# Kernel optimization log

Measured on AMD Instinct MI355X. Metric: run time of the kernel, lower is better.

The kernel has to match this reference:

```python
import math
import jax, jax.numpy as jnp
import numpy as np

FACTOR = 5

def setup_inputs() -> dict:
    key = jax.random.key(0)
    kq, kk, kv, ki = jax.random.split(key, 4)
    b, h, L, d = 4, 8, 4096, 64
    sample_k = min(L, int(FACTOR * math.log(L + 1)))  # 41
    q = jax.random.normal(kq, (b, h, L, d), dtype=jnp.float32)
    k = jax.random.normal(kk, (b, h, L, d), dtype=jnp.float32)
    v = jax.random.normal(kv, (b, h, L, d), dtype=jnp.float32)
    index_sample = jax.random.randint(ki, (L, sample_k), 0, L, dtype=jnp.int64)
    return {"q": q, "k": k, "v": v, "index_sample": index_sample}

def reference(q, k, v, index_sample):
    b, h, l_q, d = q.shape
    l_k = k.shape[2]
    n_top = min(l_q, int(FACTOR * math.log(l_q + 1)))
    # --- ProbSparse query selection ---
    # k_sample[b,h,q,s,d] = k[b,h,index_sample[q,s],d]  (avoids the O(lq*lk*d) expand)
    k_sample = k[:, :, index_sample, :]                      # (b,h,l_q,sample_k,d)
    qk_sample = jnp.einsum('bhqd,bhqsd->bhqs', q, k_sample)  # (b,h,l_q,sample_k)
    m = qk_sample.max(axis=-1) - qk_sample.mean(axis=-1)     # sparsity measure
    _, top_q = jax.lax.top_k(m, n_top)                       # (b,h,n_top)
    # --- sparse attention on selected queries ---
    q_reduce = jnp.take_along_axis(q, top_q[..., None], axis=2)  # (b,h,n_top,d)
    scale = 1.0 / math.sqrt(d)
    scores = jnp.einsum('bhnd,bhkd->bhnk', q_reduce, k) * scale
    attn = jax.nn.softmax(scores, axis=-1)
    context_top = jnp.einsum('bhnk,bhkd->bhnd', attn, v)
    # --- scatter into mean-initialized context (attn_mask is None path) ---
    context = jnp.broadcast_to(v.mean(axis=2, keepdims=True), (b, h, l_q, d))
    bi = jnp.arange(b)[:, None, None]
    hi = jnp.arange(h)[None, :, None]
    context = context.at[bi, hi, top_q].set(context_top)
    return context
```

## Files before the change

### kernel.cpp

```cpp
#include <hip/hip_runtime.h>
#include <hip/hip_bf16.h>


#define NTOP 41
#define NPAD 48
#define CH 64
#define CAND_CAP 64

typedef __attribute__((ext_vector_type(8))) short bf16x8;
typedef __attribute__((ext_vector_type(4))) float f32x4;

__device__ __forceinline__ unsigned short f2bf(float f) {
    unsigned int x = __float_as_uint(f);
    unsigned int r = (x + 0x7FFFu + ((x >> 16) & 1u)) >> 16;
    return (unsigned short)r;
}
__device__ __forceinline__ unsigned int pack2(float lo, float hi) {
    return ((unsigned int)f2bf(hi) << 16) | f2bf(lo);
}
__device__ __forceinline__ float dot8(const float4& qa, const float4& qb,
                                      const float4& ka, const float4& kb) {
    float p = 0.f;
    p = fmaf(qa.x, ka.x, p); p = fmaf(qa.y, ka.y, p);
    p = fmaf(qa.z, ka.z, p); p = fmaf(qa.w, ka.w, p);
    p = fmaf(qb.x, kb.x, p); p = fmaf(qb.y, kb.y, p);
    p = fmaf(qb.z, kb.z, p); p = fmaf(qb.w, kb.w, p);
    return p;
}
__device__ __forceinline__ float red8(float p) {
    p += __shfl_xor(p, 1);
    p += __shfl_xor(p, 2);
    p += __shfl_xor(p, 4);
    return p;
}

__global__ __launch_bounds__(256) void kA_scores(const float* __restrict__ q,
                                                 const float* __restrict__ k,
                                                 const int* __restrict__ idxs,
                                                 float* __restrict__ m_out) {
    __shared__ int sidx[32 * 41];
    int t = threadIdx.x;
    int lane = t & 63, w = t >> 6;
    int g = lane >> 3, sl = lane & 7;
    int lb = ((blockIdx.x & 7) << 9) + (blockIdx.x >> 3);
    long long qflat = (long long)lb * 32 + w * 8 + g;
    int bh = (int)(qflat >> 12);
    int qi0 = (lb * 32) & 4095;
    for (int i = t; i < 32 * 41; i += 256)
        sidx[i] = idxs[(long long)qi0 * 41 + i] & 4095;
    const float4* q4 = (const float4*)q;
    const float4* k4 = (const float4*)k;
    float4 qa = q4[qflat * 16 + sl * 2];
    float4 qb = q4[qflat * 16 + sl * 2 + 1];
    long long kbase = ((long long)bh << 12) * 16;
    __syncthreads();
    const int* irow = sidx + (w * 8 + g) * 41;
    float maxv = -1e30f, sum = 0.f;
#pragma unroll 2
    for (int g4 = 0; g4 < 10; g4++) {
        int ki0 = irow[g4 * 4 + 0], ki1 = irow[g4 * 4 + 1];
        int ki2 = irow[g4 * 4 + 2], ki3 = irow[g4 * 4 + 3];
        float4 ka0 = k4[kbase + (long long)ki0 * 16 + sl * 2];
        float4 kb0 = k4[kbase + (long long)ki0 * 16 + sl * 2 + 1];
        float4 ka1 = k4[kbase + (long long)ki1 * 16 + sl * 2];
        float4 kb1 = k4[kbase + (long long)ki1 * 16 + sl * 2 + 1];
        float4 ka2 = k4[kbase + (long long)ki2 * 16 + sl * 2];
        float4 kb2 = k4[kbase + (long long)ki2 * 16 + sl * 2 + 1];
        float4 ka3 = k4[kbase + (long long)ki3 * 16 + sl * 2];
        float4 kb3 = k4[kbase + (long long)ki3 * 16 + sl * 2 + 1];
        float p0 = red8(dot8(qa, qb, ka0, kb0));
        float p1 = red8(dot8(qa, qb, ka1, kb1));
        float p2 = red8(dot8(qa, qb, ka2, kb2));
        float p3 = red8(dot8(qa, qb, ka3, kb3));
        maxv = fmaxf(maxv, fmaxf(fmaxf(p0, p1), fmaxf(p2, p3)));
        sum += (p0 + p1) + (p2 + p3);
    }
    {
        int ki = irow[40];
        float4 ka = k4[kbase + (long long)ki * 16 + sl * 2];
        float4 kb = k4[kbase + (long long)ki * 16 + sl * 2 + 1];
        float p = red8(dot8(qa, qb, ka, kb));
        maxv = fmaxf(maxv, p);
        sum += p;
    }
    if (sl == 0) m_out[qflat] = maxv - sum * (1.0f / 41.0f);
}

__global__ __launch_bounds__(256) void kB_topk(const float* __restrict__ m_in,
                                               int* __restrict__ topq) {
    __shared__ unsigned int uvals[4096];
    __shared__ unsigned int hist[256];
    __shared__ unsigned int scal[4];
    __shared__ int candIdx[CAND_CAP];
    __shared__ unsigned int candU[CAND_CAP];
    int bh = blockIdx.x, t = threadIdx.x;
    for (int i = t; i < 4096; i += 256) {
        unsigned int b = __float_as_uint(m_in[bh * 4096 + i]);
        uvals[i] = (b & 0x80000000u) ? ~b : (b | 0x80000000u);
    }
    hist[t] = 0;
    __syncthreads();
    for (int i = t; i < 4096; i += 256) atomicAdd(&hist[uvals[i] >> 24], 1u);
    __syncthreads();
    if (t == 0) {
        unsigned int cum = 0, b1 = 0, ca = 0;
        for (int j = 255; j >= 0; j--) {
            if (cum + hist[j] >= 41u) { b1 = (unsigned)j; ca = cum; break; }
            cum += hist[j];
        }
        scal[0] = b1; scal[1] = ca;
    }
    __syncthreads();
    unsigned int b1 = scal[0];
    hist[t] = 0;
    __syncthreads();
    for (int i = t; i < 4096; i += 256)
        if ((uvals[i] >> 24) == b1) atomicAdd(&hist[(uvals[i] >> 16) & 255u], 1u);
    __syncthreads();
    if (t == 0) {
        unsigned int cum = scal[1], b2 = 0;
        for (int j = 255; j >= 0; j--) {
            if (cum + hist[j] >= 41u) { b2 = (unsigned)j; break; }
            cum += hist[j];
        }
        scal[2] = (b1 << 24) | (b2 << 16);
        scal[3] = 0;
    }
    __syncthreads();
    unsigned int T = scal[2];
    for (int i = t; i < 4096; i += 256) {
        unsigned int u = uvals[i];
        if (u >= T) {
            unsigned int pos = atomicAdd(&scal[3], 1u);
            if (pos < CAND_CAP) { candIdx[pos] = i; candU[pos] = u; }
        }
    }
    __syncthreads();
    if (t < 64) {
        int n = (int)min(scal[3], (unsigned)CAND_CAP);
        unsigned int myU = (t < n) ? candU[t] : 0u;
        int myI = (t < n) ? candIdx[t] : 0x7fffffff;
        for (int it = 0; it < NTOP; it++) {
            unsigned int bu = myU;
            int bi = myI;
            for (int off = 32; off; off >>= 1) {
                unsigned int ou = __shfl_xor(bu, off);
                int oi = __shfl_xor(bi, off);
                if (ou > bu || (ou == bu && oi < bi)) { bu = ou; bi = oi; }
            }
            if (t == 0) topq[bh * NTOP + it] = bi;
            if (myI == bi) { myU = 0u; myI = 0x7fffffff; }
        }
    }
}

__global__ __launch_bounds__(256) void kC1(const float* __restrict__ v,
                                           float* __restrict__ vpart) {
    int bh = blockIdx.x, chn = blockIdx.y, t = threadIdx.x;
    int d = t & 63, r = t >> 6;
    long long base = ((long long)bh << 12) + chn * 256;
    float acc = 0.f;
    for (int i = 0; i < 64; i++) acc += v[(base + i * 4 + r) * 64 + d];
    __shared__ float red[256];
    red[t] = acc;
    __syncthreads();
    if (r == 0) vpart[(bh * 16 + chn) * 64 + d] = red[d] + red[64 + d] + red[128 + d] + red[192 + d];
}

__global__ __launch_bounds__(256) void kD(const float* __restrict__ vpart,
                                          float* __restrict__ out) {
    __shared__ __align__(16) float vm[64];
    int t = threadIdx.x;
    int bh = blockIdx.x >> 6;
    if (t < 64) {
        float s = 0.f;
#pragma unroll
        for (int c = 0; c < 16; c++) s += vpart[(bh * 16 + c) * 64 + t];
        vm[t] = s * (1.0f / 4096.0f);
    }
    __syncthreads();
    long long g0 = (long long)blockIdx.x * 1024 + t;
    float4* out4 = (float4*)out;
#pragma unroll
    for (int i = 0; i < 4; i++) {
        long long gg = g0 + i * 256;
        int d4 = (int)(gg & 15);
        out4[gg] = *(const float4*)(&vm[d4 * 4]);
    }
}

__global__ __launch_bounds__(256) void kE_attn(const float* __restrict__ q,
                                               const float* __restrict__ k,
                                               const float* __restrict__ v,
                                               const int* __restrict__ topq,
                                               float* __restrict__ part, int tl) {
    __shared__ unsigned short qs[NPAD * 72];
    __shared__ unsigned short kb[CH * 72];
    __shared__ unsigned short vt[64 * 72];
    __shared__ unsigned short pb[NPAD * 72];
    __shared__ float sp[NPAD * 65];
    __shared__ float m_i[NPAD], l_i[NPAD], fac[NPAD];

    const int t = threadIdx.x;
    const int tile = blockIdx.x, bh = blockIdx.y;
    const int tiles = gridDim.x;
    const int lane = t & 63, w = t >> 6;
    const int c = lane & 15, quad = lane >> 4;
    const long long bhbase = ((long long)bh) << 12;

    const float4* q4f = (const float4*)q;
    const float4* k4f = (const float4*)k;
    const float4* v4f = (const float4*)v;

    for (int i = t; i < NTOP * 16; i += 256) {
        int n = i >> 4, oc = i & 15;
        int row = topq[bh * NTOP + n];
        float4 val = q4f[(bhbase + row) * 16 + oc];
        uint2 pk;
        pk.x = pack2(val.x * 0.125f, val.y * 0.125f);
        pk.y = pack2(val.z * 0.125f, val.w * 0.125f);
        *(uint2*)(&qs[n * 72 + oc * 4]) = pk;
    }
    for (int i = t; i < 7 * 72; i += 256) {
        qs[NTOP * 72 + i] = 0;
        pb[NTOP * 72 + i] = 0;
    }
    if (t < NPAD) { m_i[t] = -1e30f; l_i[t] = 0.f; fac[t] = 0.f; }

    f32x4 oacc[3];
#pragma unroll
    for (int qt = 0; qt < 3; qt++) oacc[qt] = (f32x4){0.f, 0.f, 0.f, 0.f};

    const int l0 = tile * tl;
    const int nchunk = tl >> 6;
    for (int ch = 0; ch < nchunk; ch++) {
        const int lb = l0 + ch * CH;
        __syncthreads();
#pragma unroll
        for (int i = 0; i < 4; i++) {
            int idx = i * 256 + t;
            int j = idx >> 4, oc = idx & 15;
            float4 val = k4f[(bhbase + lb + j) * 16 + oc];
            uint2 pk;
            pk.x = pack2(val.x, val.y);
            pk.y = pack2(val.z, val.w);
            *(uint2*)(&kb[j * 72 + oc * 4]) = pk;
        }
        {
            int jp = t & 31, o = t >> 5;
            float4 a0 = v4f[(bhbase + lb + 2 * jp) * 16 + o * 2];
            float4 a1 = v4f[(bhbase + lb + 2 * jp) * 16 + o * 2 + 1];
            float4 b0 = v4f[(bhbase + lb + 2 * jp + 1) * 16 + o * 2];
            float4 b1 = v4f[(bhbase + lb + 2 * jp + 1) * 16 + o * 2 + 1];
            float av[8] = {a0.x, a0.y, a0.z, a0.w, a1.x, a1.y, a1.z, a1.w};
            float bv[8] = {b0.x, b0.y, b0.z, b0.w, b1.x, b1.y, b1.z, b1.w};
#pragma unroll
            for (int e = 0; e < 8; e++)
                *(unsigned int*)(&vt[(o * 8 + e) * 72 + 2 * jp]) = pack2(av[e], bv[e]);
        }
        __syncthreads();
        {
            const bf16x8 bk0 = *(const bf16x8*)(&kb[(w * 16 + c) * 72 + quad * 8]);
            const bf16x8 bk1 = *(const bf16x8*)(&kb[(w * 16 + c) * 72 + quad * 8 + 32]);
#pragma unroll
            for (int qt = 0; qt < 3; qt++) {
                const bf16x8 a0 = *(const bf16x8*)(&qs[(qt * 16 + c) * 72 + quad * 8]);
                const bf16x8 a1 = *(const bf16x8*)(&qs[(qt * 16 + c) * 72 + quad * 8 + 32]);
                f32x4 s4 = (f32x4){0.f, 0.f, 0.f, 0.f};
                s4 = __builtin_amdgcn_mfma_f32_16x16x32_bf16(a0, bk0, s4, 0, 0, 0);
                s4 = __builtin_amdgcn_mfma_f32_16x16x32_bf16(a1, bk1, s4, 0, 0, 0);
#pragma unroll
                for (int r = 0; r < 4; r++)
                    sp[(qt * 16 + quad * 4 + r) * 65 + w * 16 + c] = s4[r];
            }
        }
        __syncthreads();
        if (t < NTOP * 4) {
            int n = t >> 2, sub = t & 3;
            float rm = -1e30f;
#pragma unroll
            for (int j = 0; j < 16; j++) rm = fmaxf(rm, sp[n * 65 + sub * 16 + j]);
            rm = fmaxf(rm, __shfl_xor(rm, 1));
            rm = fmaxf(rm, __shfl_xor(rm, 2));
            float mo = m_i[n];
            float mn = fmaxf(mo, rm);
            float ssum = 0.f;
#pragma unroll
            for (int j = 0; j < 16; j += 2) {
                float e0 = __expf(sp[n * 65 + sub * 16 + j] - mn);
                float e1 = __expf(sp[n * 65 + sub * 16 + j + 1] - mn);
                ssum += e0 + e1;
                *(unsigned int*)(&pb[n * 72 + sub * 16 + j]) = pack2(e0, e1);
            }
            ssum += __shfl_xor(ssum, 1);
            ssum += __shfl_xor(ssum, 2);
            if (sub == 0) {
                float f = __expf(mo - mn);
                fac[n] = f;
                l_i[n] = l_i[n] * f + ssum;
                m_i[n] = mn;
            }
        }
        __syncthreads();
        {
            const bf16x8 bv0 = *(const bf16x8*)(&vt[(w * 16 + c) * 72 + quad * 8]);
            const bf16x8 bv1 = *(const bf16x8*)(&vt[(w * 16 + c) * 72 + quad * 8 + 32]);
#pragma unroll
            for (int qt = 0; qt < 3; qt++) {
                const bf16x8 a0 = *(const bf16x8*)(&pb[(qt * 16 + c) * 72 + quad * 8]);
                const bf16x8 a1 = *(const bf16x8*)(&pb[(qt * 16 + c) * 72 + quad * 8 + 32]);
                f32x4 o = oacc[qt];
                o.x *= fac[qt * 16 + quad * 4 + 0];
                o.y *= fac[qt * 16 + quad * 4 + 1];
                o.z *= fac[qt * 16 + quad * 4 + 2];
                o.w *= fac[qt * 16 + quad * 4 + 3];
                o = __builtin_amdgcn_mfma_f32_16x16x32_bf16(a0, bv0, o, 0, 0, 0);
                o = __builtin_amdgcn_mfma_f32_16x16x32_bf16(a1, bv1, o, 0, 0, 0);
                oacc[qt] = o;
            }
        }
    }
    __syncthreads();
    long long pbase = ((long long)(bh * tiles + tile)) * NTOP * 66;
    if (t < NTOP) {
        part[pbase + t * 66 + 0] = m_i[t];
        part[pbase + t * 66 + 1] = l_i[t];
    }
#pragma unroll
    for (int qt = 0; qt < 3; qt++) {
#pragma unroll
        for (int r = 0; r < 4; r++) {
            int n = qt * 16 + quad * 4 + r;
            if (n < NTOP) part[pbase + (long long)n * 66 + 2 + w * 16 + c] = oacc[qt][r];
        }
    }
}

__global__ __launch_bounds__(256) void kF_combine(const float* __restrict__ part,
                                                  const int* __restrict__ topq,
                                                  float* __restrict__ out, int tiles) {
    int t = threadIdx.x;
    int bh = blockIdx.x;
    int n = blockIdx.y * 4 + (t >> 6);
    int d = t & 63;
    if (n >= NTOP) return;
    long long base = ((long long)(bh * tiles)) * NTOP * 66 + (long long)n * 66;
    const long long ts = (long long)NTOP * 66;
    float M = -1e30f;
    for (int tt = 0; tt < tiles; tt++) M = fmaxf(M, part[base + tt * ts]);
    float L = 0.f, acc = 0.f;
    for (int tt = 0; tt < tiles; tt++) {
        float mt = part[base + tt * ts];
        float wgt = __expf(mt - M);
        L += part[base + tt * ts + 1] * wgt;
        acc += part[base + tt * ts + 2 + d] * wgt;
    }
    int row = topq[bh * NTOP + n];
    out[(((long long)bh << 12) + row) * 64 + d] = acc / L;
}

extern "C" void kernel_launch(void* const* d_in, const int* in_sizes, int n_in,
                              void* d_out, int out_size, void* d_ws, size_t ws_size,
                              hipStream_t stream) {
    const float* q = (const float*)d_in[0];
    const float* k = (const float*)d_in[1];
    const float* v = (const float*)d_in[2];
    const int* idxs = (const int*)d_in[3];
    float* out = (float*)d_out;

    char* ws = (char*)d_ws;
    float* ws_m = (float*)ws;
    int* ws_topq = (int*)(ws + 524288);
    float* ws_vpart = (float*)(ws + 532480);
    float* ws_part = (float*)(ws + 671744);

    size_t need16 = 671744ull + 16ull * 32 * NTOP * 66 * 4;
    int tiles = (ws_size >= need16) ? 16 : 8;
    int tl = 4096 / tiles;

    kA_scores<<<4096, 256, 0, stream>>>(q, k, idxs, ws_m);
    kB_topk<<<32, 256, 0, stream>>>(ws_m, ws_topq);
    kC1<<<dim3(32, 16), 256, 0, stream>>>(v, ws_vpart);
    kD<<<2048, 256, 0, stream>>>(ws_vpart, out);
    kE_attn<<<dim3(tiles, 32), 256, 0, stream>>>(q, k, v, ws_topq, ws_part, tl);
    kF_combine<<<dim3(32, 11), 256, 0, stream>>>(ws_part, ws_topq, out, tiles);
}
```

Baseline: 252.1 us.

## Fuse V-sum into scoring kernel and mean broadcast into attention kernel

Merges the V column-sum kernel into the sampled-score kernel as extra blocks, and the mean-broadcast output fill into the attention kernel as extra blocks. This cuts six launches to four and lets independent work overlap within a grid. It also remaps attention blocks so the heads are spread across XCDs, unrolls the sampled-key loop to issue eight gathers at once, and adds an occupancy hint of 5 blocks per CU. The cost is more register pressure in the unrolled loop and heterogeneous blocks inside one grid.

Result: no change. 256.7 us (+1.8%).

```diff
diff --git a/kernel.cpp b/kernel.cpp
--- a/kernel.cpp
+++ b/kernel.cpp
@@ -34,15 +34,35 @@
     return p;
 }
 
-__global__ __launch_bounds__(256) void kA_scores(const float* __restrict__ q,
-                                                 const float* __restrict__ k,
-                                                 const int* __restrict__ idxs,
-                                                 float* __restrict__ m_out) {
-    __shared__ int sidx[32 * 41];
+__global__ __launch_bounds__(256, 5) void K1_scores_vsum(const float* __restrict__ q,
+                                                         const float* __restrict__ k,
+                                                         const float* __restrict__ v,
+                                                         const int* __restrict__ idxs,
+                                                         float* __restrict__ m_out,
+                                                         float* __restrict__ vpart) {
+    __shared__ __align__(16) char smem[32 * 41 * 4 > 1024 ? 32 * 41 * 4 : 1024];
     int t = threadIdx.x;
+    int bid = blockIdx.x;
+
+    if (bid < 512) {
+        float* red = (float*)smem;
+        int bh = bid >> 4, chn = bid & 15;
+        int d = t & 63, r = t >> 6;
+        long long base = ((long long)bh << 12) + chn * 256;
+        float acc = 0.f;
+        for (int i = 0; i < 64; i++) acc += v[(base + i * 4 + r) * 64 + d];
+        red[t] = acc;
+        __syncthreads();
+        if (r == 0)
+            vpart[(bh * 16 + chn) * 64 + d] = red[d] + red[64 + d] + red[128 + d] + red[192 + d];
+        return;
+    }
+
+    int* sidx = (int*)smem;
+    int abid = bid - 512;
     int lane = t & 63, w = t >> 6;
     int g = lane >> 3, sl = lane & 7;
-    int lb = ((blockIdx.x & 7) << 9) + (blockIdx.x >> 3);
+    int lb = ((abid & 7) << 9) + (abid >> 3);
     long long qflat = (long long)lb * 32 + w * 8 + g;
     int bh = (int)(qflat >> 12);
     int qi0 = (lb * 32) & 4095;
@@ -55,31 +75,33 @@
     long long kbase = ((long long)bh << 12) * 16;
     __syncthreads();
     const int* irow = sidx + (w * 8 + g) * 41;
+
+    int k40 = irow[40];
+    float4 ka40 = k4[kbase + (long long)k40 * 16 + sl * 2];
+    float4 kb40 = k4[kbase + (long long)k40 * 16 + sl * 2 + 1];
+
     float maxv = -1e30f, sum = 0.f;
-#pragma unroll 2
-    for (int g4 = 0; g4 < 10; g4++) {
-        int ki0 = irow[g4 * 4 + 0], ki1 = irow[g4 * 4 + 1];
-        int ki2 = irow[g4 * 4 + 2], ki3 = irow[g4 * 4 + 3];
-        float4 ka0 = k4[kbase + (long long)ki0 * 16 + sl * 2];
-        float4 kb0 = k4[kbase + (long long)ki0 * 16 + sl * 2 + 1];
-        float4 ka1 = k4[kbase + (long long)ki1 * 16 + sl * 2];
-        float4 kb1 = k4[kbase + (long long)ki1 * 16 + sl * 2 + 1];
-        float4 ka2 = k4[kbase + (long long)ki2 * 16 + sl * 2];
-        float4 kb2 = k4[kbase + (long long)ki2 * 16 + sl * 2 + 1];
-        float4 ka3 = k4[kbase + (long long)ki3 * 16 + sl * 2];
-        float4 kb3 = k4[kbase + (long long)ki3 * 16 + sl * 2 + 1];
-        float p0 = red8(dot8(qa, qb, ka0, kb0));
-        float p1 = red8(dot8(qa, qb, ka1, kb1));
-        float p2 = red8(dot8(qa, qb, ka2, kb2));
-        float p3 = red8(dot8(qa, qb, ka3, kb3));
-        maxv = fmaxf(maxv, fmaxf(fmaxf(p0, p1), fmaxf(p2, p3)));
-        sum += (p0 + p1) + (p2 + p3);
+#pragma unroll
+    for (int g8 = 0; g8 < 5; g8++) {
+        int kis[8];
+#pragma unroll
+        for (int u = 0; u < 8; u++) kis[u] = irow[g8 * 8 + u];
+        float4 ka[8], kb[8];
+#pragma unroll
+        for (int u = 0; u < 8; u++) {
+            long long roff = kbase + (long long)kis[u] * 16 + sl * 2;
+            ka[u] = k4[roff];
+            kb[u] = k4[roff + 1];
+        }
+#pragma unroll
+        for (int u = 0; u < 8; u++) {
+            float p = red8(dot8(qa, qb, ka[u], kb[u]));
+            maxv = fmaxf(maxv, p);
+            sum += p;
+        }
     }
     {
-        int ki = irow[40];
-        float4 ka = k4[kbase + (long long)ki * 16 + sl * 2];
-        float4 kb = k4[kbase + (long long)ki * 16 + sl * 2 + 1];
-        float p = red8(dot8(qa, qb, ka, kb));
+        float p = red8(dot8(qa, qb, ka40, kb40));
         maxv = fmaxf(maxv, p);
         sum += p;
     }
@@ -154,56 +176,49 @@
     }
 }
 
-__global__ __launch_bounds__(256) void kC1(const float* __restrict__ v,
-                                           float* __restrict__ vpart) {
-    int bh = blockIdx.x, chn = blockIdx.y, t = threadIdx.x;
-    int d = t & 63, r = t >> 6;
-    long long base = ((long long)bh << 12) + chn * 256;
-    float acc = 0.f;
-    for (int i = 0; i < 64; i++) acc += v[(base + i * 4 + r) * 64 + d];
-    __shared__ float red[256];
-    red[t] = acc;
-    __syncthreads();
-    if (r == 0) vpart[(bh * 16 + chn) * 64 + d] = red[d] + red[64 + d] + red[128 + d] + red[192 + d];
-}
-
-__global__ __launch_bounds__(256) void kD(const float* __restrict__ vpart,
-                                          float* __restrict__ out) {
-    __shared__ __align__(16) float vm[64];
-    int t = threadIdx.x;
-    int bh = blockIdx.x >> 6;
-    if (t < 64) {
-        float s = 0.f;
-#pragma unroll
-        for (int c = 0; c < 16; c++) s += vpart[(bh * 16 + c) * 64 + t];
-        vm[t] = s * (1.0f / 4096.0f);
-    }
-    __syncthreads();
-    long long g0 = (long long)blockIdx.x * 1024 + t;
-    float4* out4 = (float4*)out;
-#pragma unroll
-    for (int i = 0; i < 4; i++) {
-        long long gg = g0 + i * 256;
-        int d4 = (int)(gg & 15);
-        out4[gg] = *(const float4*)(&vm[d4 * 4]);
-    }
-}
-
-__global__ __launch_bounds__(256) void kE_attn(const float* __restrict__ q,
-                                               const float* __restrict__ k,
-                                               const float* __restrict__ v,
-                                               const int* __restrict__ topq,
-                                               float* __restrict__ part, int tl) {
+__global__ __launch_bounds__(256) void K3_attn_bcast(const float* __restrict__ q,
+                                                     const float* __restrict__ k,
+                                                     const float* __restrict__ v,
+                                                     const int* __restrict__ topq,
+                                                     const float* __restrict__ vpart,
+                                                     float* __restrict__ part,
+                                                     float* __restrict__ out,
+                                                     int tiles, int tl) {
     __shared__ unsigned short qs[NPAD * 72];
     __shared__ unsigned short kb[CH * 72];
     __shared__ unsigned short vt[64 * 72];
     __shared__ unsigned short pb[NPAD * 72];
     __shared__ float sp[NPAD * 65];
     __shared__ float m_i[NPAD], l_i[NPAD], fac[NPAD];
+    __shared__ __align__(16) float vm[64];
 
     const int t = threadIdx.x;
-    const int tile = blockIdx.x, bh = blockIdx.y;
-    const int tiles = gridDim.x;
+    const int bid = blockIdx.x;
+    const int nE = tiles * 32;
+
+    if (bid >= nE) {
+        int gb = bid - nE;
+        int bh = gb >> 6;
+        if (t < 64) {
+            float s = 0.f;
+#pragma unroll
+            for (int c = 0; c < 16; c++) s += vpart[(bh * 16 + c) * 64 + t];
+            vm[t] = s * (1.0f / 4096.0f);
+        }
+        __syncthreads();
+        long long g0 = (long long)gb * 1024 + t;
+        float4* out4 = (float4*)out;
+#pragma unroll
+        for (int i = 0; i < 4; i++) {
+            long long gg = g0 + i * 256;
+            int d4 = (int)(gg & 15);
+            out4[gg] = *(const float4*)(&vm[d4 * 4]);
+        }
+        return;
+    }
+
+    const int xcd = bid & 7, sub = (bid >> 3) & 3, tile = bid >> 5;
+    const int bh = (xcd << 2) | sub;
     const int lane = t & 63, w = t >> 6;
     const int c = lane & 15, quad = lane >> 4;
     const long long bhbase = ((long long)bh) << 12;
@@ -276,10 +291,10 @@
         }
         __syncthreads();
         if (t < NTOP * 4) {
-            int n = t >> 2, sub = t & 3;
+            int n = t >> 2, sub2 = t & 3;
             float rm = -1e30f;
 #pragma unroll
-            for (int j = 0; j < 16; j++) rm = fmaxf(rm, sp[n * 65 + sub * 16 + j]);
+            for (int j = 0; j < 16; j++) rm = fmaxf(rm, sp[n * 65 + sub2 * 16 + j]);
             rm = fmaxf(rm, __shfl_xor(rm, 1));
             rm = fmaxf(rm, __shfl_xor(rm, 2));
             float mo = m_i[n];
@@ -287,14 +302,14 @@
             float ssum = 0.f;
 #pragma unroll
             for (int j = 0; j < 16; j += 2) {
-                float e0 = __expf(sp[n * 65 + sub * 16 + j] - mn);
-                float e1 = __expf(sp[n * 65 + sub * 16 + j + 1] - mn);
+                float e0 = __expf(sp[n * 65 + sub2 * 16 + j] - mn);
+                float e1 = __expf(sp[n * 65 + sub2 * 16 + j + 1] - mn);
                 ssum += e0 + e1;
-                *(unsigned int*)(&pb[n * 72 + sub * 16 + j]) = pack2(e0, e1);
+                *(unsigned int*)(&pb[n * 72 + sub2 * 16 + j]) = pack2(e0, e1);
             }
             ssum += __shfl_xor(ssum, 1);
             ssum += __shfl_xor(ssum, 2);
-            if (sub == 0) {
+            if (sub2 == 0) {
                 float f = __expf(mo - mn);
                 fac[n] = f;
                 l_i[n] = l_i[n] * f + ssum;
@@ -378,10 +393,9 @@
     int tiles = (ws_size >= need16) ? 16 : 8;
     int tl = 4096 / tiles;
 
-    kA_scores<<<4096, 256, 0, stream>>>(q, k, idxs, ws_m);
+    K1_scores_vsum<<<512 + 4096, 256, 0, stream>>>(q, k, v, idxs, ws_m, ws_vpart);
     kB_topk<<<32, 256, 0, stream>>>(ws_m, ws_topq);
-    kC1<<<dim3(32, 16), 256, 0, stream>>>(v, ws_vpart);
-    kD<<<2048, 256, 0, stream>>>(ws_vpart, out);
-    kE_attn<<<dim3(tiles, 32), 256, 0, stream>>>(q, k, v, ws_topq, ws_part, tl);
+    K3_attn_bcast<<<tiles * 32 + 2048, 256, 0, stream>>>(q, k, v, ws_topq, ws_vpart,
+                                                         ws_part, out, tiles, tl);
     kF_combine<<<dim3(32, 11), 256, 0, stream>>>(ws_part, ws_topq, out, tiles);
 }
```

## Do online softmax in registers with wave shuffles; alias workspace buffers

Applied to the files above, without the earlier changes.

The attention kernel no longer writes QK scores to a shared score buffer and re-reads them for the softmax. Row max and row sum are now reduced in registers with cross-lane shuffles, and only per-wave partials go through small shared arrays. Probabilities are written as bf16 into the K tile buffer, replacing the separate P buffer and cutting LDS use and traffic. The workspace is repacked so the sparsity-score buffer shares space with the partial-result buffer, which lowers the size needed for the 16-tile split. The cost is an extra barrier per chunk and more shuffle instructions.

Result: slower. 266.4 us (+5.7%).

```diff
diff --git a/kernel.cpp b/kernel.cpp
--- a/kernel.cpp
+++ b/kernel.cpp
@@ -195,10 +195,10 @@
                                                const int* __restrict__ topq,
                                                float* __restrict__ part, int tl) {
     __shared__ unsigned short qs[NPAD * 72];
-    __shared__ unsigned short kb[CH * 72];
+    __shared__ unsigned short kpb[CH * 72];
     __shared__ unsigned short vt[64 * 72];
-    __shared__ unsigned short pb[NPAD * 72];
-    __shared__ float sp[NPAD * 65];
+    __shared__ float redM[NPAD * 4];
+    __shared__ float redS[NPAD * 4];
     __shared__ float m_i[NPAD], l_i[NPAD], fac[NPAD];
 
     const int t = threadIdx.x;
@@ -221,10 +221,7 @@
         pk.y = pack2(val.z * 0.125f, val.w * 0.125f);
         *(uint2*)(&qs[n * 72 + oc * 4]) = pk;
     }
-    for (int i = t; i < 7 * 72; i += 256) {
-        qs[NTOP * 72 + i] = 0;
-        pb[NTOP * 72 + i] = 0;
-    }
+    for (int i = t; i < 7 * 72; i += 256) qs[NTOP * 72 + i] = 0;
     if (t < NPAD) { m_i[t] = -1e30f; l_i[t] = 0.f; fac[t] = 0.f; }
 
     f32x4 oacc[3];
@@ -244,7 +241,7 @@
             uint2 pk;
             pk.x = pack2(val.x, val.y);
             pk.y = pack2(val.z, val.w);
-            *(uint2*)(&kb[j * 72 + oc * 4]) = pk;
+            *(uint2*)(&kpb[j * 72 + oc * 4]) = pk;
         }
         {
             int jp = t & 31, o = t >> 5;
@@ -259,9 +256,10 @@
                 *(unsigned int*)(&vt[(o * 8 + e) * 72 + 2 * jp]) = pack2(av[e], bv[e]);
         }
         __syncthreads();
+        f32x4 s[3];
         {
-            const bf16x8 bk0 = *(const bf16x8*)(&kb[(w * 16 + c) * 72 + quad * 8]);
-            const bf16x8 bk1 = *(const bf16x8*)(&kb[(w * 16 + c) * 72 + quad * 8 + 32]);
+            const bf16x8 bk0 = *(const bf16x8*)(&kpb[(w * 16 + c) * 72 + quad * 8]);
+            const bf16x8 bk1 = *(const bf16x8*)(&kpb[(w * 16 + c) * 72 + quad * 8 + 32]);
 #pragma unroll
             for (int qt = 0; qt < 3; qt++) {
                 const bf16x8 a0 = *(const bf16x8*)(&qs[(qt * 16 + c) * 72 + quad * 8]);
@@ -269,46 +267,59 @@
                 f32x4 s4 = (f32x4){0.f, 0.f, 0.f, 0.f};
                 s4 = __builtin_amdgcn_mfma_f32_16x16x32_bf16(a0, bk0, s4, 0, 0, 0);
                 s4 = __builtin_amdgcn_mfma_f32_16x16x32_bf16(a1, bk1, s4, 0, 0, 0);
-#pragma unroll
-                for (int r = 0; r < 4; r++)
-                    sp[(qt * 16 + quad * 4 + r) * 65 + w * 16 + c] = s4[r];
-            }
-        }
-        __syncthreads();
-        if (t < NTOP * 4) {
-            int n = t >> 2, sub = t & 3;
-            float rm = -1e30f;
-#pragma unroll
-            for (int j = 0; j < 16; j++) rm = fmaxf(rm, sp[n * 65 + sub * 16 + j]);
-            rm = fmaxf(rm, __shfl_xor(rm, 1));
-            rm = fmaxf(rm, __shfl_xor(rm, 2));
-            float mo = m_i[n];
+                s[qt] = s4;
+            }
+        }
+#pragma unroll
+        for (int qt = 0; qt < 3; qt++) {
+#pragma unroll
+            for (int r = 0; r < 4; r++) {
+                float x = s[qt][r];
+                x = fmaxf(x, __shfl_xor(x, 1));
+                x = fmaxf(x, __shfl_xor(x, 2));
+                x = fmaxf(x, __shfl_xor(x, 4));
+                x = fmaxf(x, __shfl_xor(x, 8));
+                if (c == 0) redM[(qt * 16 + quad * 4 + r) * 4 + w] = x;
+            }
+        }
+        __syncthreads();
+        if (t < NPAD) {
+            float rm = fmaxf(fmaxf(redM[t * 4], redM[t * 4 + 1]),
+                             fmaxf(redM[t * 4 + 2], redM[t * 4 + 3]));
+            float mo = m_i[t];
             float mn = fmaxf(mo, rm);
-            float ssum = 0.f;
-#pragma unroll
-            for (int j = 0; j < 16; j += 2) {
-                float e0 = __expf(sp[n * 65 + sub * 16 + j] - mn);
-                float e1 = __expf(sp[n * 65 + sub * 16 + j + 1] - mn);
-                ssum += e0 + e1;
-                *(unsigned int*)(&pb[n * 72 + sub * 16 + j]) = pack2(e0, e1);
-            }
-            ssum += __shfl_xor(ssum, 1);
-            ssum += __shfl_xor(ssum, 2);
-            if (sub == 0) {
-                float f = __expf(mo - mn);
-                fac[n] = f;
-                l_i[n] = l_i[n] * f + ssum;
-                m_i[n] = mn;
-            }
-        }
-        __syncthreads();
+            fac[t] = __expf(mo - mn);
+            m_i[t] = mn;
+        }
+        __syncthreads();
+#pragma unroll
+        for (int qt = 0; qt < 3; qt++) {
+#pragma unroll
+            for (int r = 0; r < 4; r++) {
+                int row = qt * 16 + quad * 4 + r;
+                float e = __expf(s[qt][r] - m_i[row]);
+                float en = __shfl_xor(e, 1);
+                if ((c & 1) == 0)
+                    *(unsigned int*)(&kpb[row * 72 + w * 16 + c]) = pack2(e, en);
+                float sm = e;
+                sm += __shfl_xor(sm, 1);
+                sm += __shfl_xor(sm, 2);
+                sm += __shfl_xor(sm, 4);
+                sm += __shfl_xor(sm, 8);
+                if (c == 0) redS[row * 4 + w] = sm;
+            }
+        }
+        __syncthreads();
+        if (t < NPAD)
+            l_i[t] = l_i[t] * fac[t] +
+                     (redS[t * 4] + redS[t * 4 + 1]) + (redS[t * 4 + 2] + redS[t * 4 + 3]);
         {
             const bf16x8 bv0 = *(const bf16x8*)(&vt[(w * 16 + c) * 72 + quad * 8]);
             const bf16x8 bv1 = *(const bf16x8*)(&vt[(w * 16 + c) * 72 + quad * 8 + 32]);
 #pragma unroll
             for (int qt = 0; qt < 3; qt++) {
-                const bf16x8 a0 = *(const bf16x8*)(&pb[(qt * 16 + c) * 72 + quad * 8]);
-                const bf16x8 a1 = *(const bf16x8*)(&pb[(qt * 16 + c) * 72 + quad * 8 + 32]);
+                const bf16x8 a0 = *(const bf16x8*)(&kpb[(qt * 16 + c) * 72 + quad * 8]);
+                const bf16x8 a1 = *(const bf16x8*)(&kpb[(qt * 16 + c) * 72 + quad * 8 + 32]);
                 f32x4 o = oacc[qt];
                 o.x *= fac[qt * 16 + quad * 4 + 0];
                 o.y *= fac[qt * 16 + quad * 4 + 1];
@@ -369,12 +380,12 @@
     float* out = (float*)d_out;
 
     char* ws = (char*)d_ws;
-    float* ws_m = (float*)ws;
-    int* ws_topq = (int*)(ws + 524288);
-    float* ws_vpart = (float*)(ws + 532480);
-    float* ws_part = (float*)(ws + 671744);
-
-    size_t need16 = 671744ull + 16ull * 32 * NTOP * 66 * 4;
+    int* ws_topq = (int*)ws;
+    float* ws_vpart = (float*)(ws + 8192);
+    float* ws_m = (float*)(ws + 147456);
+    float* ws_part = (float*)(ws + 147456);
+
+    size_t need16 = 147456ull + 16ull * 32 * NTOP * 66 * 4;
     int tiles = (ws_size >= need16) ? 16 : 8;
     int tl = 4096 / tiles;
 
```
